# Performance work log

Hardware: AMD Instinct MI355X
Metric: run time of the kernel (lower is better)

## Reference

```python
import jax, jax.numpy as jnp
import numpy as np

ALPHA = 0.2  # leaky relu slope
NEG_INF = -1.0e12


def _gat(x, adj, W, a):
    # x: [N, Fin], W: [Fin, Fout], a: [2*Fout, 1]
    h = x @ W                                  # [N, Fout]
    Fout = W.shape[1]
    # additive attention: e_ij = leakyrelu(h_i . a[:Fout] + h_j . a[Fout:])
    f1 = h @ a[:Fout, 0]                       # [N]
    f2 = h @ a[Fout:, 0]                       # [N]
    e = jax.nn.leaky_relu(f1[:, None] + f2[None, :], ALPHA)  # [N, N]
    att = jnp.where(adj > 0, e, NEG_INF)
    att = jax.nn.softmax(att, axis=1)          # dropout=0 -> identity
    return jax.nn.elu(att @ h + h)             # [N, Fout]


def setup_inputs() -> dict:
    key = jax.random.key(0)
    k = jax.random.split(key, 6)
    N, NFEAT, NHID, NNEXT = 8192, 256, 128, 1024
    x = jax.random.normal(k[0], (N, NFEAT), dtype=jnp.float32)
    adj = (jax.random.uniform(k[1], (N, N)) > 0.9).astype(jnp.float32)
    # xavier-uniform-ish init
    def xav(kk, shape):
        lim = np.sqrt(6.0 / (shape[0] + shape[1])) * 1.414
        return jax.random.uniform(kk, shape, minval=-lim, maxval=lim, dtype=jnp.float32)
    W_embed = xav(k[2], (NFEAT, NHID))
    a_embed = xav(k[3], (2 * NHID, 1))
    W_assign = xav(k[4], (NFEAT, NNEXT))
    a_assign = xav(k[5], (2 * NNEXT, 1))
    return {"x": x, "adj": adj, "W_embed": W_embed, "a_embed": a_embed,
            "W_assign": W_assign, "a_assign": a_assign}


def reference(x, adj, W_embed, a_embed, W_assign, a_assign):
    z_l = _gat(x, adj, W_embed, a_embed)          # [N, nhid]
    assign = _gat(x, adj, W_assign, a_assign)     # [N, nnext]
    s_l = jax.nn.softmax(assign, axis=-1)         # [N, nnext]
    xnext = s_l.T @ z_l                            # [nnext, nhid]
    anext = s_l.T @ adj @ s_l                      # [nnext, nnext]
    return xnext, anext, s_l
```

## Files before the change

### kernel.cpp

```cpp
#include <hip/hip_runtime.h>
#include <hip/hip_bf16.h>


#define DI __device__ __forceinline__

typedef __attribute__((ext_vector_type(8))) short short8;
typedef __attribute__((ext_vector_type(4))) float f32x4;

static DI float bf2f(short s) {
    union { unsigned u; float f; } c;
    c.u = ((unsigned)(unsigned short)s) << 16;
    return c.f;
}
static DI short f2bf(float f) {
    union { float f; unsigned u; } c; c.f = f;
    unsigned r = (c.u + 0x7FFFu + ((c.u >> 16) & 1u)) >> 16;
    return (short)(unsigned short)r;
}
template <int F32>
static DI short8 ld8(const void* base, size_t off) {
    if (F32 == 0) return *(const short8*)((const short*)base + off);
    const float* p = (const float*)base + off;
    f32x4 a = *(const f32x4*)p;
    f32x4 b = *(const f32x4*)(p + 4);
    short8 v;
    #pragma unroll
    for (int e = 0; e < 4; e++) { v[e] = f2bf(a[e]); v[4 + e] = f2bf(b[e]); }
    return v;
}
static DI float wred_sum(float v) {
    #pragma unroll
    for (int o = 32; o > 0; o >>= 1) v += __shfl_down(v, o, 64);
    return v;
}
static DI float wred_max(float v) {
    #pragma unroll
    for (int o = 32; o > 0; o >>= 1) v = fmaxf(v, __shfl_down(v, o, 64));
    return v;
}
static DI int sfun(int r) { return (r ^ (r >> 3)) & 7; }
static DI int swzk(int k, int r) {
    return (k & ~63) | ((((k >> 3) & 7) ^ sfun(r)) << 3) | (k & 7);
}
static DI unsigned pack2(short lo, short hi) {
    return ((unsigned)(unsigned short)lo) | (((unsigned)(unsigned short)hi) << 16);
}
static DI void gload16(const void* g, void* l) {
    __builtin_amdgcn_global_load_lds(
        (const __attribute__((address_space(1))) unsigned int*)g,
        (__attribute__((address_space(3))) unsigned int*)l, 16, 0, 0);
}

template <int EPI, int SWZX>
__launch_bounds__(256)
__global__ void gemm_lds(const short* __restrict__ A, const short* __restrict__ Bt,
                         void* __restrict__ C, int ldc, int kcount) {
    __shared__ short As0[128][64], Bs0[128][64];
    __shared__ short As1[128][64], Bs1[128][64];
    int bx = blockIdx.x, by = blockIdx.y;
    if (SWZX) {
        int lid = blockIdx.x + blockIdx.y * 8;
        int c = lid & 7, s = lid >> 3;
        by = c * 8 + (s >> 3);
        bx = s & 7;
    }
    const int tid  = threadIdx.x;
    const int lane = tid & 63;
    const int w    = tid >> 6;
    const int wr   = w >> 1, wc = w & 1;
    const int i0   = by * 128;
    const int n0   = bx * 128;
    const int k0   = blockIdx.z * kcount;

    const int srow = w * 32 + (lane >> 3);
    const short* gA = A  + (size_t)(i0 + srow) * 8192 + k0 + (lane & 7) * 8;
    const short* gB = Bt + (size_t)(n0 + srow) * 8192 + k0 + (lane & 7) * 8;

    f32x4 acc[4][4];
    #pragma unroll
    for (int m = 0; m < 4; m++)
        #pragma unroll
        for (int n = 0; n < 4; n++) acc[m][n] = (f32x4){0.f, 0.f, 0.f, 0.f};

#define STAGE_TILE(ts, Ab, Bb)                                                  \
    do {                                                                        \
        _Pragma("unroll")                                                       \
        for (int j = 0; j < 4; j++) {                                           \
            gload16(gA + (size_t)(ts) * 64 + (size_t)j * 8 * 8192,              \
                    &Ab[w * 32 + j * 8][0]);                                    \
            gload16(gB + (size_t)(ts) * 64 + (size_t)j * 8 * 8192,              \
                    &Bb[w * 32 + j * 8][0]);                                    \
        }                                                                       \
    } while (0)

#define COMPUTE_TILE(Ab, Bb)                                                    \
    do {                                                                        \
        _Pragma("unroll")                                                       \
        for (int kk = 0; kk < 2; kk++) {                                        \
            short8 af[4], bq[4];                                                \
            _Pragma("unroll")                                                   \
            for (int m = 0; m < 4; m++) {                                       \
                int ar = wr * 64 + m * 16 + (lane & 15);                        \
                af[m] = *(const short8*)&Ab[ar]                                 \
                            [swzk(kk * 32 + (lane >> 4) * 8, ar)];              \
            }                                                                   \
            _Pragma("unroll")                                                   \
            for (int n = 0; n < 4; n++) {                                       \
                int br = wc * 64 + n * 16 + (lane & 15);                        \
                bq[n] = *(const short8*)&Bb[br]                                 \
                            [swzk(kk * 32 + (lane >> 4) * 8, br)];              \
            }                                                                   \
            _Pragma("unroll")                                                   \
            for (int m = 0; m < 4; m++)                                         \
                _Pragma("unroll")                                               \
                for (int n = 0; n < 4; n++)                                     \
                    acc[m][n] = __builtin_amdgcn_mfma_f32_16x16x32_bf16(        \
                        af[m], bq[n], acc[m][n], 0, 0, 0);                      \
        }                                                                       \
    } while (0)

    const int nt = kcount >> 6;
    STAGE_TILE(0, As0, Bs0);
    for (int t = 0; t < nt; t += 2) {
        __syncthreads();
        STAGE_TILE(t + 1, As1, Bs1);
        COMPUTE_TILE(As0, Bs0);
        __syncthreads();
        if (t + 2 < nt) STAGE_TILE(t + 2, As0, Bs0);
        COMPUTE_TILE(As1, Bs1);
    }
#undef STAGE_TILE

    #pragma unroll
    for (int m = 0; m < 4; m++) {
        #pragma unroll
        for (int n = 0; n < 4; n++) {
            int row0 = i0 + wr * 64 + m * 16 + ((lane >> 4) << 2);
            int col  = n0 + wc * 64 + n * 16 + (lane & 15);
            if (EPI == 1) {
                unsigned long long pk = 0;
                #pragma unroll
                for (int r = 0; r < 4; r++)
                    pk |= (unsigned long long)(unsigned short)f2bf(acc[m][n][r])
                          << (16 * r);
                *(unsigned long long*)((short*)C + (size_t)col * 8192 +
                                       swzk(row0, col)) = pk;
            } else {
                #pragma unroll
                for (int r = 0; r < 4; r++) {
                    float v = acc[m][n][r];
                    if (EPI == 0) ((float*)C)[(size_t)(row0 + r) * ldc + col] = v;
                    else atomicAdd(&((float*)C)[(size_t)(row0 + r) * ldc + col], v);
                }
            }
        }
    }
#undef COMPUTE_TILE
}

template <int EPI, int GEN, int SWZX>
__launch_bounds__(256)
__global__ void gemm_gen(const short* __restrict__ Ab, const short* __restrict__ Bt,
                         void* __restrict__ C, int ldc, int kcount,
                         const float* __restrict__ E1, const float* __restrict__ F1,
                         const float* __restrict__ E2, const float* __restrict__ F2) {
    __shared__ short As0[128][64], Bs0[128][64];
    __shared__ short As1[128][64], Bs1[128][64];
    int bx = blockIdx.x, by = blockIdx.y;
    if (SWZX) {
        int lid = blockIdx.x + blockIdx.y * 8;
        int c = lid & 7, s = lid >> 3;
        by = c * 8 + (s >> 3);
        bx = s & 7;
    }
    const int tid  = threadIdx.x;
    const int lane = tid & 63;
    const int w    = tid >> 6;
    const int wr   = w >> 1, wc = w & 1;
    const int i0   = by * 128;
    const int n0   = bx * 128;
    const int k0   = blockIdx.z * kcount;

    const int srow = w * 32 + (lane >> 3);
    const short* gB = Bt + (size_t)(n0 + srow) * 8192 + k0 + (lane & 7) * 8;

    f32x4 acc[4][4];
    #pragma unroll
    for (int m = 0; m < 4; m++)
        #pragma unroll
        for (int n = 0; n < 4; n++) acc[m][n] = (f32x4){0.f, 0.f, 0.f, 0.f};

    short8 avr[4];

#define G_ALOAD(ts)                                                             \
    do {                                                                        \
        _Pragma("unroll")                                                       \
        for (int it = 0; it < 4; it++) {                                        \
            int idx = it * 256 + tid;                                           \
            int r = idx >> 3, kb = idx & 7;                                     \
            avr[it] = *(const short8*)(Ab + (size_t)(i0 + r) * 8192 + k0 +      \
                                       (size_t)(ts) * 64 + kb * 8);             \
        }                                                                       \
    } while (0)

#define G_BLOAD(ts, Bb)                                                         \
    do {                                                                        \
        _Pragma("unroll")                                                       \
        for (int j = 0; j < 4; j++)                                             \
            gload16(gB + (size_t)(ts) * 64 + (size_t)j * 8 * 8192,              \
                    &Bb[w * 32 + j * 8][0]);                                    \
    } while (0)

#define G_WSTAGE(ts, As_)                                                       \
    do {                                                                        \
        _Pragma("unroll")                                                       \
        for (int it = 0; it < 4; it++) {                                        \
            int idx = it * 256 + tid;                                           \
            int r = idx >> 3, kb = idx & 7;                                     \
            short8 av = avr[it], p;                                             \
            if (GEN == 1) {                                                     \
                _Pragma("unroll")                                               \
                for (int e = 0; e < 8; e++)                                     \
                    p[e] = ((unsigned short)av[e]) ? (short)0x3F80 : (short)0;  \
            } else {                                                            \
                int kl = k0 + (ts) * 64 + ((kb ^ sfun(r)) << 3);                \
                float e1r = E1[i0 + r], f1r = F1[i0 + r];                       \
                f32x4 e2a = *(const f32x4*)(E2 + kl);                           \
                f32x4 e2b = *(const f32x4*)(E2 + kl + 4);                       \
                f32x4 f2a = *(const f32x4*)(F2 + kl);                           \
                f32x4 f2b = *(const f32x4*)(F2 + kl + 4);                       \
                _Pragma("unroll")                                               \
                for (int e = 0; e < 8; e++) {                                   \
                    float ev = e < 4 ? e2a[e] : e2b[e - 4];                     \
                    float fv = e < 4 ? f2a[e] : f2b[e - 4];                     \
                    float wg = fmaxf(e1r * ev, f1r * fv);                       \
                    p[e] = ((unsigned short)av[e]) ? f2bf(wg) : (short)0;       \
                }                                                               \
            }                                                                   \
            *(short8*)&As_[r][kb * 8] = p;                                      \
        }                                                                       \
    } while (0)

#define G_COMPUTE(Ab_, Bb_)                                                     \
    do {                                                                        \
        _Pragma("unroll")                                                       \
        for (int kk = 0; kk < 2; kk++) {                                        \
            short8 af[4], bq[4];                                                \
            _Pragma("unroll")                                                   \
            for (int m = 0; m < 4; m++) {                                       \
                int ar = wr * 64 + m * 16 + (lane & 15);                        \
                af[m] = *(const short8*)&Ab_[ar]                                \
                            [swzk(kk * 32 + (lane >> 4) * 8, ar)];              \
            }                                                                   \
            _Pragma("unroll")                                                   \
            for (int n = 0; n < 4; n++) {                                       \
                int br = wc * 64 + n * 16 + (lane & 15);                        \
                bq[n] = *(const short8*)&Bb_[br]                                \
                            [swzk(kk * 32 + (lane >> 4) * 8, br)];              \
            }                                                                   \
            _Pragma("unroll")                                                   \
            for (int m = 0; m < 4; m++)                                         \
                _Pragma("unroll")                                               \
                for (int n = 0; n < 4; n++)                                     \
                    acc[m][n] = __builtin_amdgcn_mfma_f32_16x16x32_bf16(        \
                        af[m], bq[n], acc[m][n], 0, 0, 0);                      \
        }                                                                       \
    } while (0)

    const int nt = kcount >> 6;
    G_ALOAD(0);
    G_BLOAD(0, Bs0);
    for (int t = 0; t < nt; t += 2) {
        G_WSTAGE(t, As0);
        __syncthreads();
        G_ALOAD(t + 1);
        G_BLOAD(t + 1, Bs1);
        G_COMPUTE(As0, Bs0);
        G_WSTAGE(t + 1, As1);
        __syncthreads();
        if (t + 2 < nt) { G_ALOAD(t + 2); G_BLOAD(t + 2, Bs0); }
        G_COMPUTE(As1, Bs1);
    }
#undef G_ALOAD
#undef G_BLOAD
#undef G_WSTAGE
#undef G_COMPUTE

    #pragma unroll
    for (int m = 0; m < 4; m++) {
        #pragma unroll
        for (int n = 0; n < 4; n++) {
            int row0 = i0 + wr * 64 + m * 16 + ((lane >> 4) << 2);
            int col  = n0 + wc * 64 + n * 16 + (lane & 15);
            if (EPI == 1) {
                unsigned long long pk = 0;
                #pragma unroll
                for (int r = 0; r < 4; r++)
                    pk |= (unsigned long long)(unsigned short)f2bf(acc[m][n][r])
                          << (16 * r);
                *(unsigned long long*)((short*)C + (size_t)col * 8192 +
                                       swzk(row0, col)) = pk;
            } else {
                #pragma unroll
                for (int r = 0; r < 4; r++)
                    atomicAdd(&((float*)C)[(size_t)(row0 + r) * ldc + col],
                              acc[m][n][r]);
            }
        }
    }
}

template <int SWZX>
__launch_bounds__(256)
__global__ void gemm_xw_k(const float* __restrict__ A, const float* __restrict__ B,
                          short* __restrict__ C, short* __restrict__ Ct, int ldn) {
    __shared__ short As[128][64];
    __shared__ short Bs[128][64];
    int bx = blockIdx.x, by = blockIdx.y;
    if (SWZX) {
        int lid = blockIdx.x + blockIdx.y * 8;
        int c = lid & 7, s = lid >> 3;
        by = c * 8 + (s >> 3);
        bx = s & 7;
    }
    const int tid  = threadIdx.x;
    const int lane = tid & 63;
    const int w    = tid >> 6;
    const int wr   = w >> 1, wc = w & 1;
    const int i0   = by * 128;
    const int n0   = bx * 128;

    f32x4 acc[4][4];
    #pragma unroll
    for (int m = 0; m < 4; m++)
        #pragma unroll
        for (int n = 0; n < 4; n++) acc[m][n] = (f32x4){0.f, 0.f, 0.f, 0.f};

    for (int ks = 0; ks < 256; ks += 64) {
        __syncthreads();
        #pragma unroll
        for (int it = 0; it < 4; it++) {
            int idx = it * 256 + tid;
            int cg = idx & 7, r = idx >> 3;
            *(short8*)&As[r][swzk(cg * 8, r)] =
                ld8<1>(A, (size_t)(i0 + r) * 256 + ks + cg * 8);
        }
        #pragma unroll
        for (int it = 0; it < 2; it++) {
            int idx = it * 256 + tid;
            int ng = idx & 15, kp = idx >> 4;
            int k = 2 * kp;
            short8 r0 = ld8<1>(B, (size_t)(ks + k) * ldn + n0 + ng * 8);
            short8 r1 = ld8<1>(B, (size_t)(ks + k + 1) * ldn + n0 + ng * 8);
            #pragma unroll
            for (int j = 0; j < 8; j++) {
                int row = ng * 8 + j;
                *(unsigned*)&Bs[row][swzk(k, row)] = pack2(r0[j], r1[j]);
            }
        }
        __syncthreads();
        #pragma unroll
        for (int kk = 0; kk < 2; kk++) {
            short8 af[4], bq[4];
            #pragma unroll
            for (int m = 0; m < 4; m++) {
                int ar = wr * 64 + m * 16 + (lane & 15);
                af[m] = *(const short8*)&As[ar][swzk(kk * 32 + (lane >> 4) * 8, ar)];
            }
            #pragma unroll
            for (int n = 0; n < 4; n++) {
                int br = wc * 64 + n * 16 + (lane & 15);
                bq[n] = *(const short8*)&Bs[br][swzk(kk * 32 + (lane >> 4) * 8, br)];
            }
            #pragma unroll
            for (int m = 0; m < 4; m++)
                #pragma unroll
                for (int n = 0; n < 4; n++)
                    acc[m][n] = __builtin_amdgcn_mfma_f32_16x16x32_bf16(
                        af[m], bq[n], acc[m][n], 0, 0, 0);
        }
    }
    #pragma unroll
    for (int m = 0; m < 4; m++) {
        #pragma unroll
        for (int n = 0; n < 4; n++) {
            int row0 = i0 + wr * 64 + m * 16 + ((lane >> 4) << 2);
            int col  = n0 + wc * 64 + n * 16 + (lane & 15);
            unsigned long long pk = 0;
            #pragma unroll
            for (int r = 0; r < 4; r++) {
                short b = f2bf(acc[m][n][r]);
                C[(size_t)(row0 + r) * ldn + col] = b;
                pk |= (unsigned long long)(unsigned short)b << (16 * r);
            }
            *(unsigned long long*)(Ct + (size_t)col * 8192 + swzk(row0, col)) = pk;
        }
    }
}

__launch_bounds__(256)
__global__ void compute_f_k(const short* __restrict__ h1, const short* __restrict__ h2,
                            const float* __restrict__ ae, const float* __restrict__ aa,
                            float* __restrict__ f11, float* __restrict__ f21,
                            float* __restrict__ f12, float* __restrict__ f22) {
    int row = blockIdx.x, t = threadIdx.x;
    float s11 = 0.f, s21 = 0.f, s12 = 0.f, s22 = 0.f;
    if (t < 128) {
        float hv = bf2f(h1[(size_t)row * 128 + t]);
        s11 = hv * ae[t];
        s21 = hv * ae[128 + t];
    }
    #pragma unroll
    for (int q = 0; q < 4; q++) {
        int f = t + q * 256;
        float hv = bf2f(h2[(size_t)row * 1024 + f]);
        s12 += hv * aa[f];
        s22 += hv * aa[1024 + f];
    }
    __shared__ float red[4][4];
    s11 = wred_sum(s11); s21 = wred_sum(s21);
    s12 = wred_sum(s12); s22 = wred_sum(s22);
    int w = t >> 6;
    if ((t & 63) == 0) { red[0][w] = s11; red[1][w] = s21; red[2][w] = s12; red[3][w] = s22; }
    __syncthreads();
    if (t == 0) {
        f11[row] = red[0][0] + red[0][1] + red[0][2] + red[0][3];
        f21[row] = red[1][0] + red[1][1] + red[1][2] + red[1][3];
        f12[row] = red[2][0] + red[2][1] + red[2][2] + red[2][3];
        f22[row] = red[3][0] + red[3][1] + red[3][2] + red[3][3];
    }
}

__launch_bounds__(256)
__global__ void evec_k(const float* __restrict__ f11, const float* __restrict__ f21,
                       const float* __restrict__ f12, const float* __restrict__ f22,
                       float* __restrict__ E11, float* __restrict__ F11,
                       float* __restrict__ E21, float* __restrict__ F21,
                       float* __restrict__ E12, float* __restrict__ F12,
                       float* __restrict__ E22, float* __restrict__ F22) {
    int i = blockIdx.x * 256 + threadIdx.x;
    if (i >= 8192) return;
    float a = f11[i], b = f21[i], c = f12[i], d = f22[i];
    E11[i] = __expf(a); F11[i] = __expf(0.2f * a);
    E21[i] = __expf(b); F21[i] = __expf(0.2f * b);
    E12[i] = __expf(c); F12[i] = __expf(0.2f * c);
    E22[i] = __expf(d); F22[i] = __expf(0.2f * d);
}

__launch_bounds__(256)
__global__ void prepass_k(const float* __restrict__ adj,
                          const float* __restrict__ E11, const float* __restrict__ F11,
                          const float* __restrict__ E21, const float* __restrict__ F21,
                          const float* __restrict__ E12, const float* __restrict__ F12,
                          const float* __restrict__ E22, const float* __restrict__ F22,
                          float* __restrict__ den1, float* __restrict__ den2,
                          short* __restrict__ P2b) {
    int row = blockIdx.x, t = threadIdx.x;
    float e1r = E11[row], f1r = F11[row];
    float e2r = E12[row], f2r = F12[row];
    float d1 = 0.f, d2 = 0.f;
    const float* arow = adj + (size_t)row * 8192;
    #pragma unroll
    for (int it = 0; it < 4; it++) {
        int jb = (it * 256 + t) * 8;
        size_t wo = (size_t)row * 8192 + swzk(jb, row);
        f32x4 a0 = *(const f32x4*)(arow + jb), a1 = *(const f32x4*)(arow + jb + 4);
        f32x4 eA0 = *(const f32x4*)(E21 + jb), eA1 = *(const f32x4*)(E21 + jb + 4);
        f32x4 fA0 = *(const f32x4*)(F21 + jb), fA1 = *(const f32x4*)(F21 + jb + 4);
        f32x4 eB0 = *(const f32x4*)(E22 + jb), eB1 = *(const f32x4*)(E22 + jb + 4);
        f32x4 fB0 = *(const f32x4*)(F22 + jb), fB1 = *(const f32x4*)(F22 + jb + 4);
        short8 p2v;
        #pragma unroll
        for (int e = 0; e < 8; e++) {
            float av = e < 4 ? a0[e] : a1[e - 4];
            float eA = e < 4 ? eA0[e] : eA1[e - 4];
            float fA = e < 4 ? fA0[e] : fA1[e - 4];
            float eB = e < 4 ? eB0[e] : eB1[e - 4];
            float fB = e < 4 ? fB0[e] : fB1[e - 4];
            float x1 = fmaxf(e1r * eA, f1r * fA);
            float x2 = fmaxf(e2r * eB, f2r * fB);
            float p1 = av > 0.f ? x1 : 0.f;
            float p2 = av > 0.f ? x2 : 0.f;
            d1 += p1; d2 += p2;
            p2v[e] = f2bf(p2);
        }
        *(short8*)(P2b + wo) = p2v;
    }
    __shared__ float r1[4], r2[4];
    d1 = wred_sum(d1); d2 = wred_sum(d2);
    if ((t & 63) == 0) { r1[t >> 6] = d1; r2[t >> 6] = d2; }
    __syncthreads();
    if (t == 0) {
        den1[row] = r1[0] + r1[1] + r1[2] + r1[3];
        den2[row] = r2[0] + r2[1] + r2[2] + r2[3];
    }
}

__launch_bounds__(256)
__global__ void epi_gat1t_k(const float* __restrict__ Y1, const float* __restrict__ den1,
                            const short* __restrict__ h1, short* __restrict__ zlt) {
    __shared__ short ts[128][65];
    int tr = blockIdx.x * 64;
    int t = threadIdx.x;
    #pragma unroll
    for (int it = 0; it < 4; it++) {
        int idx = it * 256 + t;
        int r = idx >> 4, cb = idx & 15;
        int row = tr + r;
        float d = den1[row]; d = d > 0.f ? d : 1.f;
        const float* yp = Y1 + (size_t)row * 128 + cb * 8;
        f32x4 y0 = *(const f32x4*)yp, y1 = *(const f32x4*)(yp + 4);
        short8 hv = *(const short8*)(h1 + (size_t)row * 128 + cb * 8);
        #pragma unroll
        for (int e = 0; e < 8; e++) {
            float z = (e < 4 ? y0[e] : y1[e - 4]) / d + bf2f(hv[e]);
            z = z > 0.f ? z : (__expf(z) - 1.f);
            ts[cb * 8 + e][r] = f2bf(z);
        }
    }
    __syncthreads();
    #pragma unroll
    for (int it = 0; it < 4; it++) {
        int idx = it * 256 + t;
        int c = idx >> 3, rb = idx & 7;
        short8 v = *(const short8*)&ts[c][rb * 8];
        *(short8*)(zlt + (size_t)c * 8192 + tr + ((rb ^ sfun(c)) << 3)) = v;
    }
}

__launch_bounds__(256)
__global__ void episoft_k(const float* __restrict__ Y2, const float* __restrict__ den2,
                          const short* __restrict__ h2, float* __restrict__ slo,
                          short* __restrict__ slb) {
    int row = blockIdx.x, t = threadIdx.x;
    float d = den2[row];
    d = d > 0.f ? d : 1.f;
    float v[4], mx = -1e30f;
    #pragma unroll
    for (int q = 0; q < 4; q++) {
        int j = t + q * 256;
        float a = Y2[(size_t)row * 1024 + j] / d + bf2f(h2[(size_t)row * 1024 + j]);
        a = a > 0.f ? a : (__expf(a) - 1.f);
        v[q] = a;
        mx = fmaxf(mx, a);
    }
    __shared__ float sred[4];
    __shared__ float sbc;
    mx = wred_max(mx);
    if ((t & 63) == 0) sred[t >> 6] = mx;
    __syncthreads();
    if (t == 0) sbc = fmaxf(fmaxf(sred[0], sred[1]), fmaxf(sred[2], sred[3]));
    __syncthreads();
    mx = sbc;
    float s = 0.f;
    #pragma unroll
    for (int q = 0; q < 4; q++) { v[q] = __expf(v[q] - mx); s += v[q]; }
    s = wred_sum(s);
    if ((t & 63) == 0) sred[t >> 6] = s;
    __syncthreads();
    if (t == 0) sbc = sred[0] + sred[1] + sred[2] + sred[3];
    __syncthreads();
    float inv = 1.f / sbc;
    #pragma unroll
    for (int q = 0; q < 4; q++) {
        float sv = v[q] * inv;
        slo[(size_t)row * 1024 + t + q * 256] = sv;
        slb[(size_t)row * 1024 + t + q * 256] = f2bf(sv);
    }
}

template <int F32IN>
__launch_bounds__(256)
__global__ void transpose_swz_k(const void* __restrict__ in, short* __restrict__ out,
                                int R, int C) {
    __shared__ short ts[64][72];
    int tc = blockIdx.x * 64;
    int tr = blockIdx.y * 64;
    int t = threadIdx.x;
    #pragma unroll
    for (int h = 0; h < 2; h++) {
        int r = (t >> 3) + h * 32, c = (t & 7) * 8;
        *(short8*)&ts[r][c] = ld8<F32IN>(in, (size_t)(tr + r) * C + tc + c);
    }
    __syncthreads();
    #pragma unroll
    for (int h = 0; h < 2; h++) {
        int n = t >> 2, blk = (t & 3) + h * 4;
        short8 v;
        #pragma unroll
        for (int e = 0; e < 8; e++) v[e] = ts[blk * 8 + e][n];
        *(short8*)(out + (size_t)(tc + n) * R + tr + ((blk ^ sfun(tc + n)) << 3)) = v;
    }
}

extern "C" void kernel_launch(void* const* d_in, const int* in_sizes, int n_in,
                              void* d_out, int out_size, void* d_ws, size_t ws_size,
                              hipStream_t stream) {
    const float* x   = (const float*)d_in[0];
    const float* adj = (const float*)d_in[1];
    const float* We  = (const float*)d_in[2];
    const float* ae  = (const float*)d_in[3];
    const float* Wa  = (const float*)d_in[4];
    const float* aa  = (const float*)d_in[5];
    float* out = (float*)d_out;

    char* w = (char*)d_ws;
    short* h1b = (short*)(w);
    short* h2b = (short*)(w + (2u   << 20));
    float* f11 = (float*)(w + (18u  << 20));
    float* f21 = f11 + 8192;  float* f12 = f21 + 8192; float* f22 = f12 + 8192;
    float* den1 = f22 + 8192; float* den2 = den1 + 8192;
    float* E11 = den2 + 8192; float* F11 = E11 + 8192;
    float* E21 = F11 + 8192;  float* F21 = E21 + 8192;
    float* E12 = F21 + 8192;  float* F12 = E12 + 8192;
    float* E22 = F12 + 8192;  float* F22 = E22 + 8192;
    float* Y1f = (float*)(w + (21u << 20));
    float* Y2f = (float*)(w + (25u << 20));
    short* slb = (short*)(w + (57u << 20));
    short* h1t = (short*)(w + (73u << 20));
    short* h2t = (short*)(w + (75u << 20));
    short* slt = (short*)(w + (91u << 20));
    short* zlt = (short*)(w + (107u << 20));
    short* tT  = (short*)(w + (109u << 20));
    short* P2b = (short*)(w + (128u << 20));

    float* xo  = out;
    float* ao  = out + 131072;
    float* slo = out + 131072 + 1048576;

    hipMemsetAsync(out, 0, (size_t)(131072 + 1048576) * 4, stream);
    hipMemsetAsync(Y1f, 0, (size_t)8192 * 128 * 4, stream);

    gemm_xw_k<0><<<dim3(1, 64), 256, 0, stream>>>(x, We, h1b, h1t, 128);
    gemm_xw_k<1><<<dim3(8, 64), 256, 0, stream>>>(x, Wa, h2b, h2t, 1024);
    compute_f_k<<<dim3(8192), 256, 0, stream>>>(h1b, h2b, ae, aa, f11, f21, f12, f22);
    evec_k<<<dim3(32), 256, 0, stream>>>(f11, f21, f12, f22,
        E11, F11, E21, F21, E12, F12, E22, F22);
    prepass_k<<<dim3(8192), 256, 0, stream>>>(adj,
        E11, F11, E21, F21, E12, F12, E22, F22, den1, den2, P2b);

    gemm_gen<3, 0, 0><<<dim3(1, 64, 8), 256, 0, stream>>>(
        P2b, h1t, Y1f, 128, 1024, E11, F11, E21, F21);
    epi_gat1t_k<<<dim3(128), 256, 0, stream>>>(Y1f, den1, h1b, zlt);

    gemm_lds<0, 1><<<dim3(8, 64, 1), 256, 0, stream>>>(P2b, h2t, Y2f, 1024, 8192);
    episoft_k<<<dim3(8192), 256, 0, stream>>>(Y2f, den2, h2b, slo, slb);
    transpose_swz_k<0><<<dim3(16, 128), 256, 0, stream>>>(slb, slt, 8192, 1024);

    gemm_gen<1, 1, 1><<<dim3(8, 64, 1), 256, 0, stream>>>(
        P2b, slt, tT, 0, 8192, nullptr, nullptr, nullptr, nullptr);

    gemm_lds<3, 0><<<dim3(8, 8, 8), 256, 0, stream>>>(slt, tT, ao, 1024, 1024);
    gemm_lds<3, 0><<<dim3(1, 8, 32), 256, 0, stream>>>(slt, zlt, xo, 128, 256);
}
```

Baseline: 721.2 us.

## Pack adjacency into a bitmask and expand it in-register inside GEMMs

```diff
diff --git a/kernel.cpp b/kernel.cpp
--- a/kernel.cpp
+++ b/kernel.cpp
@@ -130,6 +130,7 @@
         COMPUTE_TILE(As1, Bs1);
     }
 #undef STAGE_TILE
+#undef COMPUTE_TILE
 
     #pragma unroll
     for (int m = 0; m < 4; m++) {
@@ -155,13 +156,113 @@
             }
         }
     }
-#undef COMPUTE_TILE
-}
-
-template <int EPI, int GEN, int SWZX>
-__launch_bounds__(256)
-__global__ void gemm_gen(const short* __restrict__ Ab, const short* __restrict__ Bt,
-                         void* __restrict__ C, int ldc, int kcount,
+}
+
+template <int SWZX>
+__launch_bounds__(256)
+__global__ void gemm_bin(const unsigned char* __restrict__ adjm,
+                         const short* __restrict__ Bt,
+                         short* __restrict__ C, int kcount) {
+    __shared__ short Bs0[128][64], Bs1[128][64];
+    __shared__ unsigned char Ms0[128][8], Ms1[128][8];
+    int bx = blockIdx.x, by = blockIdx.y;
+    if (SWZX) {
+        int lid = blockIdx.x + blockIdx.y * 8;
+        int c = lid & 7, s = lid >> 3;
+        by = c * 8 + (s >> 3);
+        bx = s & 7;
+    }
+    const int tid  = threadIdx.x;
+    const int lane = tid & 63;
+    const int w    = tid >> 6;
+    const int wr   = w >> 1, wc = w & 1;
+    const int i0   = by * 128;
+    const int n0   = bx * 128;
+    const int k0   = blockIdx.z * kcount;
+
+    const int srow = w * 32 + (lane >> 3);
+    const short* gB = Bt + (size_t)(n0 + srow) * 8192 + k0 + (lane & 7) * 8;
+    const unsigned char* gM = adjm + (size_t)(i0 + (tid >> 1)) * 1024 +
+                              (k0 >> 3) + (tid & 1) * 4;
+
+    f32x4 acc[4][4];
+    #pragma unroll
+    for (int m = 0; m < 4; m++)
+        #pragma unroll
+        for (int n = 0; n < 4; n++) acc[m][n] = (f32x4){0.f, 0.f, 0.f, 0.f};
+
+#define BN_STAGE(ts, Bb, Mb)                                                    \
+    do {                                                                        \
+        _Pragma("unroll")                                                       \
+        for (int j = 0; j < 4; j++)                                             \
+            gload16(gB + (size_t)(ts) * 64 + (size_t)j * 8 * 8192,              \
+                    &Bb[w * 32 + j * 8][0]);                                    \
+        unsigned mv = *(const unsigned*)(gM + (size_t)(ts) * 8);                \
+        *(unsigned*)&Mb[tid >> 1][(tid & 1) * 4] = mv;                          \
+    } while (0)
+
+#define BN_COMPUTE(Bb, Mb)                                                      \
+    do {                                                                        \
+        _Pragma("unroll")                                                       \
+        for (int kk = 0; kk < 2; kk++) {                                        \
+            short8 af[4], bq[4];                                                \
+            _Pragma("unroll")                                                   \
+            for (int m = 0; m < 4; m++) {                                       \
+                int ar = wr * 64 + m * 16 + (lane & 15);                        \
+                unsigned mbyte = Mb[ar][kk * 4 + (lane >> 4)];                  \
+                _Pragma("unroll")                                               \
+                for (int e = 0; e < 8; e++)                                     \
+                    af[m][e] = ((mbyte >> e) & 1) ? (short)0x3F80 : (short)0;   \
+            }                                                                   \
+            _Pragma("unroll")                                                   \
+            for (int n = 0; n < 4; n++) {                                       \
+                int br = wc * 64 + n * 16 + (lane & 15);                        \
+                bq[n] = *(const short8*)&Bb[br]                                 \
+                            [swzk(kk * 32 + (lane >> 4) * 8, br)];              \
+            }                                                                   \
+            _Pragma("unroll")                                                   \
+            for (int m = 0; m < 4; m++)                                         \
+                _Pragma("unroll")                                               \
+                for (int n = 0; n < 4; n++)                                     \
+                    acc[m][n] = __builtin_amdgcn_mfma_f32_16x16x32_bf16(        \
+                        af[m], bq[n], acc[m][n], 0, 0, 0);                      \
+        }                                                                       \
+    } while (0)
+
+    const int nt = kcount >> 6;
+    BN_STAGE(0, Bs0, Ms0);
+    for (int t = 0; t < nt; t += 2) {
+        __syncthreads();
+        BN_STAGE(t + 1, Bs1, Ms1);
+        BN_COMPUTE(Bs0, Ms0);
+        __syncthreads();
+        if (t + 2 < nt) BN_STAGE(t + 2, Bs0, Ms0);
+        BN_COMPUTE(Bs1, Ms1);
+    }
+#undef BN_STAGE
+#undef BN_COMPUTE
+
+    #pragma unroll
+    for (int m = 0; m < 4; m++) {
+        #pragma unroll
+        for (int n = 0; n < 4; n++) {
+            int row0 = i0 + wr * 64 + m * 16 + ((lane >> 4) << 2);
+            int col  = n0 + wc * 64 + n * 16 + (lane & 15);
+            unsigned long long pk = 0;
+            #pragma unroll
+            for (int r = 0; r < 4; r++)
+                pk |= (unsigned long long)(unsigned short)f2bf(acc[m][n][r])
+                      << (16 * r);
+            *(unsigned long long*)(C + (size_t)col * 8192 + swzk(row0, col)) = pk;
+        }
+    }
+}
+
+template <int EPI, int SWZX>
+__launch_bounds__(256)
+__global__ void gemm_gen(const unsigned char* __restrict__ adjm,
+                         const short* __restrict__ Bt,
+                         float* __restrict__ C, int ldc, int kcount,
                          const float* __restrict__ E1, const float* __restrict__ F1,
                          const float* __restrict__ E2, const float* __restrict__ F2) {
     __shared__ short As0[128][64], Bs0[128][64];
@@ -183,6 +284,9 @@
 
     const int srow = w * 32 + (lane >> 3);
     const short* gB = Bt + (size_t)(n0 + srow) * 8192 + k0 + (lane & 7) * 8;
+    const int mr = tid >> 1, mh = tid & 1;
+    const unsigned char* gM = adjm + (size_t)(i0 + mr) * 1024 + (k0 >> 3) + mh * 4;
+    const float e1v = E1[i0 + mr], f1v = F1[i0 + mr];
 
     f32x4 acc[4][4];
     #pragma unroll
@@ -190,18 +294,10 @@
         #pragma unroll
         for (int n = 0; n < 4; n++) acc[m][n] = (f32x4){0.f, 0.f, 0.f, 0.f};
 
-    short8 avr[4];
+    unsigned mreg;
 
 #define G_ALOAD(ts)                                                             \
-    do {                                                                        \
-        _Pragma("unroll")                                                       \
-        for (int it = 0; it < 4; it++) {                                        \
-            int idx = it * 256 + tid;                                           \
-            int r = idx >> 3, kb = idx & 7;                                     \
-            avr[it] = *(const short8*)(Ab + (size_t)(i0 + r) * 8192 + k0 +      \
-                                       (size_t)(ts) * 64 + kb * 8);             \
-        }                                                                       \
-    } while (0)
+    do { mreg = *(const unsigned*)(gM + (size_t)(ts) * 8); } while (0)
 
 #define G_BLOAD(ts, Bb)                                                         \
     do {                                                                        \
@@ -214,30 +310,23 @@
 #define G_WSTAGE(ts, As_)                                                       \
     do {                                                                        \
         _Pragma("unroll")                                                       \
-        for (int it = 0; it < 4; it++) {                                        \
-            int idx = it * 256 + tid;                                           \
-            int r = idx >> 3, kb = idx & 7;                                     \
-            short8 av = avr[it], p;                                             \
-            if (GEN == 1) {                                                     \
-                _Pragma("unroll")                                               \
-                for (int e = 0; e < 8; e++)                                     \
-                    p[e] = ((unsigned short)av[e]) ? (short)0x3F80 : (short)0;  \
-            } else {                                                            \
-                int kl = k0 + (ts) * 64 + ((kb ^ sfun(r)) << 3);                \
-                float e1r = E1[i0 + r], f1r = F1[i0 + r];                       \
-                f32x4 e2a = *(const f32x4*)(E2 + kl);                           \
-                f32x4 e2b = *(const f32x4*)(E2 + kl + 4);                       \
-                f32x4 f2a = *(const f32x4*)(F2 + kl);                           \
-                f32x4 f2b = *(const f32x4*)(F2 + kl + 4);                       \
-                _Pragma("unroll")                                               \
-                for (int e = 0; e < 8; e++) {                                   \
-                    float ev = e < 4 ? e2a[e] : e2b[e - 4];                     \
-                    float fv = e < 4 ? f2a[e] : f2b[e - 4];                     \
-                    float wg = fmaxf(e1r * ev, f1r * fv);                       \
-                    p[e] = ((unsigned short)av[e]) ? f2bf(wg) : (short)0;       \
-                }                                                               \
+        for (int b = 0; b < 4; b++) {                                           \
+            int kbr = mh * 4 + b;                                               \
+            int rk = k0 + (ts) * 64 + kbr * 8;                                  \
+            unsigned mbyte = (mreg >> (8 * b)) & 0xFFu;                         \
+            f32x4 e2a = *(const f32x4*)(E2 + rk);                               \
+            f32x4 e2b = *(const f32x4*)(E2 + rk + 4);                           \
+            f32x4 f2a = *(const f32x4*)(F2 + rk);                               \
+            f32x4 f2b = *(const f32x4*)(F2 + rk + 4);                           \
+            short8 p;                                                           \
+            _Pragma("unroll")                                                   \
+            for (int e = 0; e < 8; e++) {                                       \
+                float ev = e < 4 ? e2a[e] : e2b[e - 4];                         \
+                float fv = e < 4 ? f2a[e] : f2b[e - 4];                         \
+                float wg = fmaxf(e1v * ev, f1v * fv);                           \
+                p[e] = ((mbyte >> e) & 1) ? f2bf(wg) : (short)0;                \
             }                                                                   \
-            *(short8*)&As_[r][kb * 8] = p;                                      \
+            *(short8*)&As_[mr][(kbr ^ sfun(mr)) * 8] = p;                       \
         }                                                                       \
     } while (0)
 
@@ -292,20 +381,9 @@
         for (int n = 0; n < 4; n++) {
             int row0 = i0 + wr * 64 + m * 16 + ((lane >> 4) << 2);
             int col  = n0 + wc * 64 + n * 16 + (lane & 15);
-            if (EPI == 1) {
-                unsigned long long pk = 0;
-                #pragma unroll
-                for (int r = 0; r < 4; r++)
-                    pk |= (unsigned long long)(unsigned short)f2bf(acc[m][n][r])
-                          << (16 * r);
-                *(unsigned long long*)((short*)C + (size_t)col * 8192 +
-                                       swzk(row0, col)) = pk;
-            } else {
-                #pragma unroll
-                for (int r = 0; r < 4; r++)
-                    atomicAdd(&((float*)C)[(size_t)(row0 + r) * ldc + col],
-                              acc[m][n][r]);
-            }
+            #pragma unroll
+            for (int r = 0; r < 4; r++)
+                atomicAdd(&C[(size_t)(row0 + r) * ldc + col], acc[m][n][r]);
         }
     }
 }
@@ -454,45 +532,58 @@
                           const float* __restrict__ E12, const float* __restrict__ F12,
                           const float* __restrict__ E22, const float* __restrict__ F22,
                           float* __restrict__ den1, float* __restrict__ den2,
-                          short* __restrict__ P2b) {
-    int row = blockIdx.x, t = threadIdx.x;
-    float e1r = E11[row], f1r = F11[row];
-    float e2r = E12[row], f2r = F12[row];
-    float d1 = 0.f, d2 = 0.f;
-    const float* arow = adj + (size_t)row * 8192;
-    #pragma unroll
-    for (int it = 0; it < 4; it++) {
-        int jb = (it * 256 + t) * 8;
-        size_t wo = (size_t)row * 8192 + swzk(jb, row);
-        f32x4 a0 = *(const f32x4*)(arow + jb), a1 = *(const f32x4*)(arow + jb + 4);
+                          short* __restrict__ P2b, unsigned char* __restrict__ adjm) {
+    const int r0 = blockIdx.x * 4, t = threadIdx.x;
+    float e1r[4], f1r[4], e2r[4], f2r[4];
+    #pragma unroll
+    for (int r = 0; r < 4; r++) {
+        e1r[r] = E11[r0 + r]; f1r[r] = F11[r0 + r];
+        e2r[r] = E12[r0 + r]; f2r[r] = F12[r0 + r];
+    }
+    float d1[4] = {0.f, 0.f, 0.f, 0.f}, d2[4] = {0.f, 0.f, 0.f, 0.f};
+    #pragma unroll
+    for (int jc = 0; jc < 4; jc++) {
+        int jb = jc * 2048 + t * 8;
         f32x4 eA0 = *(const f32x4*)(E21 + jb), eA1 = *(const f32x4*)(E21 + jb + 4);
         f32x4 fA0 = *(const f32x4*)(F21 + jb), fA1 = *(const f32x4*)(F21 + jb + 4);
         f32x4 eB0 = *(const f32x4*)(E22 + jb), eB1 = *(const f32x4*)(E22 + jb + 4);
         f32x4 fB0 = *(const f32x4*)(F22 + jb), fB1 = *(const f32x4*)(F22 + jb + 4);
-        short8 p2v;
-        #pragma unroll
-        for (int e = 0; e < 8; e++) {
-            float av = e < 4 ? a0[e] : a1[e - 4];
-            float eA = e < 4 ? eA0[e] : eA1[e - 4];
-            float fA = e < 4 ? fA0[e] : fA1[e - 4];
-            float eB = e < 4 ? eB0[e] : eB1[e - 4];
-            float fB = e < 4 ? fB0[e] : fB1[e - 4];
-            float x1 = fmaxf(e1r * eA, f1r * fA);
-            float x2 = fmaxf(e2r * eB, f2r * fB);
-            float p1 = av > 0.f ? x1 : 0.f;
-            float p2 = av > 0.f ? x2 : 0.f;
-            d1 += p1; d2 += p2;
-            p2v[e] = f2bf(p2);
-        }
-        *(short8*)(P2b + wo) = p2v;
-    }
-    __shared__ float r1[4], r2[4];
-    d1 = wred_sum(d1); d2 = wred_sum(d2);
-    if ((t & 63) == 0) { r1[t >> 6] = d1; r2[t >> 6] = d2; }
+        #pragma unroll
+        for (int r = 0; r < 4; r++) {
+            const float* ap = adj + (size_t)(r0 + r) * 8192 + jb;
+            f32x4 a0 = *(const f32x4*)ap, a1 = *(const f32x4*)(ap + 4);
+            short8 p2v;
+            unsigned mb = 0;
+            #pragma unroll
+            for (int e = 0; e < 8; e++) {
+                float av = e < 4 ? a0[e] : a1[e - 4];
+                float eA = e < 4 ? eA0[e] : eA1[e - 4];
+                float fA = e < 4 ? fA0[e] : fA1[e - 4];
+                float eB = e < 4 ? eB0[e] : eB1[e - 4];
+                float fB = e < 4 ? fB0[e] : fB1[e - 4];
+                float x1 = fmaxf(e1r[r] * eA, f1r[r] * fA);
+                float x2 = fmaxf(e2r[r] * eB, f2r[r] * fB);
+                bool on = av > 0.f;
+                d1[r] += on ? x1 : 0.f;
+                d2[r] += on ? x2 : 0.f;
+                p2v[e] = on ? f2bf(x2) : (short)0;
+                mb |= (on ? 1u : 0u) << e;
+            }
+            *(short8*)(P2b + (size_t)(r0 + r) * 8192 + swzk(jb, r0 + r)) = p2v;
+            adjm[(size_t)(r0 + r) * 1024 + (jb >> 3)] = (unsigned char)mb;
+        }
+    }
+    __shared__ float r1s[4][4], r2s[4][4];
+    #pragma unroll
+    for (int r = 0; r < 4; r++) { d1[r] = wred_sum(d1[r]); d2[r] = wred_sum(d2[r]); }
+    if ((t & 63) == 0) {
+        #pragma unroll
+        for (int r = 0; r < 4; r++) { r1s[t >> 6][r] = d1[r]; r2s[t >> 6][r] = d2[r]; }
+    }
     __syncthreads();
-    if (t == 0) {
-        den1[row] = r1[0] + r1[1] + r1[2] + r1[3];
-        den2[row] = r2[0] + r2[1] + r2[2] + r2[3];
+    if (t < 4) {
+        den1[r0 + t] = r1s[0][t] + r1s[1][t] + r1s[2][t] + r1s[3][t];
+        den2[r0 + t] = r2s[0][t] + r2s[1][t] + r2s[2][t] + r2s[3][t];
     }
 }
 
@@ -623,6 +714,7 @@
     short* zlt = (short*)(w + (107u << 20));
     short* tT  = (short*)(w + (109u << 20));
     short* P2b = (short*)(w + (128u << 20));
+    unsigned char* adjm = (unsigned char*)(w + (256u << 20));
 
     float* xo  = out;
     float* ao  = out + 131072;
@@ -636,19 +728,18 @@
     compute_f_k<<<dim3(8192), 256, 0, stream>>>(h1b, h2b, ae, aa, f11, f21, f12, f22);
     evec_k<<<dim3(32), 256, 0, stream>>>(f11, f21, f12, f22,
         E11, F11, E21, F21, E12, F12, E22, F22);
-    prepass_k<<<dim3(8192), 256, 0, stream>>>(adj,
-        E11, F11, E21, F21, E12, F12, E22, F22, den1, den2, P2b);
-
-    gemm_gen<3, 0, 0><<<dim3(1, 64, 8), 256, 0, stream>>>(
-        P2b, h1t, Y1f, 128, 1024, E11, F11, E21, F21);
+    prepass_k<<<dim3(2048), 256, 0, stream>>>(adj,
+        E11, F11, E21, F21, E12, F12, E22, F22, den1, den2, P2b, adjm);
+
+    gemm_gen<3, 0><<<dim3(1, 64, 8), 256, 0, stream>>>(
+        adjm, h1t, Y1f, 128, 1024, E11, F11, E21, F21);
     epi_gat1t_k<<<dim3(128), 256, 0, stream>>>(Y1f, den1, h1b, zlt);
 
     gemm_lds<0, 1><<<dim3(8, 64, 1), 256, 0, stream>>>(P2b, h2t, Y2f, 1024, 8192);
     episoft_k<<<dim3(8192), 256, 0, stream>>>(Y2f, den2, h2b, slo, slb);
     transpose_swz_k<0><<<dim3(16, 128), 256, 0, stream>>>(slb, slt, 8192, 1024);
 
-    gemm_gen<1, 1, 1><<<dim3(8, 64, 1), 256, 0, stream>>>(
-        P2b, slt, tT, 0, 8192, nullptr, nullptr, nullptr, nullptr);
+    gemm_bin<1><<<dim3(8, 64, 1), 256, 0, stream>>>(adjm, slt, tT, 8192);
 
     gemm_lds<3, 0><<<dim3(8, 8, 8), 256, 0, stream>>>(slt, tT, ao, 1024, 1024);
     gemm_lds<3, 0><<<dim3(1, 8, 32), 256, 0, stream>>>(slt, zlt, xo, 128, 256);
```

Result: no change. 708.5 us (-1.8%).
